# Kernel tuning notes

Measured on AMD Instinct MI355X. Metric: run time of the kernel, lower is better.

Reference implementation:

```python
import jax, jax.numpy as jnp
import numpy as np

DIM = 512
HEADS = 8
NUM_KEYS = 256
TOPK = 32
DIM_HEAD = 128
LN_EPS = 1e-5


def setup_inputs() -> dict:
    key = jax.random.key(0)
    k1, k2, k3, k4 = jax.random.split(key, 4)
    b, t = 2, 1024
    dim_query = DIM_HEAD * HEADS * 2
    x = jax.random.normal(k1, (b, t, DIM), dtype=jnp.float32)
    # nn.Linear(dim, dim_query, bias=False): weight (dim_query, dim), default kaiming-ish; use scaled normal
    Wq = jax.random.normal(k2, (dim_query, DIM), dtype=jnp.float32) / np.sqrt(DIM)
    # keys: (heads, num_keys, 2, dim_head), std = 1/sqrt(dim_head)
    keys = jax.random.normal(k3, (HEADS, NUM_KEYS, 2, DIM_HEAD), dtype=jnp.float32) / np.sqrt(DIM_HEAD)
    # values: (num_keys**2, dim), std = 1/sqrt(dim)
    values = jax.random.normal(k4, (NUM_KEYS ** 2, DIM), dtype=jnp.float32) / np.sqrt(DIM)
    ln_gamma = jnp.ones((DIM_HEAD,), dtype=jnp.float32)
    ln_beta = jnp.zeros((DIM_HEAD,), dtype=jnp.float32)
    return {"x": x, "Wq": Wq, "keys": keys, "values": values,
            "ln_gamma": ln_gamma, "ln_beta": ln_beta}


def reference(x, Wq, keys, values, ln_gamma, ln_beta):
    b, t, _ = x.shape
    h, n, _, d = keys.shape  # (heads, num_keys, 2, dim_head)
    k = TOPK

    # queries: 'b t (p h d)' -> (b, t, 2, h, d)
    q = jnp.einsum('btc,qc->btq', x, Wq).reshape(b, t, 2, h, d)

    # LayerNorm over dim_head (use_layernorm=True path)
    mu = q.mean(axis=-1, keepdims=True)
    var = q.var(axis=-1, keepdims=True)
    q = (q - mu) * jax.lax.rsqrt(var + LN_EPS) * ln_gamma + ln_beta

    # dots: 'p b t h d, h n p d -> b t h p n'
    dots = jnp.einsum('btphd,hnpd->bthpn', q, keys)

    # top-k per sub-key half: (b, t, h, 2, k)
    scores, indices = jax.lax.top_k(dots, k)
    sx, sy = scores[..., 0, :], scores[..., 1, :]
    ix, iy = indices[..., 0, :], indices[..., 1, :]

    # outer combination -> (b, t, h, k*k)
    all_scores = (sx[..., :, None] + sy[..., None, :]).reshape(b, t, h, k * k)
    all_indices = (ix[..., :, None] * n + iy[..., None, :]).reshape(b, t, h, k * k)

    final_scores, final_idx = jax.lax.top_k(all_scores, k)  # (b, t, h, k)
    value_indices = jnp.take_along_axis(all_indices, final_idx, axis=-1)
    attn = jax.nn.softmax(final_scores, axis=-1)

    vi = value_indices.reshape(b * t, h * k)
    w = attn.reshape(b * t, h * k)

    # EmbeddingBag(mode='sum') with per-sample weights
    gathered = values[vi]                      # (bt, hk, dim)
    out = jnp.einsum('nkd,nk->nd', gathered, w)
    return out.reshape(b, t, -1)
```

## Files before the change

kernel.cpp:

```cpp
#include <hip/hip_runtime.h>
#include <math.h>

#define DQ 2048
#define CDIM 512
#define NKEYS 256
#define KSEL 32

__device__ __forceinline__ bool rank_before(float as, int ai, float bs, int bi) {
  return (as > bs) || (as == bs && ai < bi);
}
static __device__ __forceinline__ float bf2f(unsigned int u) {
  union { unsigned int i; float f; } v; v.i = u << 16; return v.f;
}
static __device__ __forceinline__ unsigned int f2bf(float f) {
  union { float f; unsigned int i; } v; v.f = f;
  unsigned int r = v.i + 0x7fffu + ((v.i >> 16) & 1u);
  return r >> 16;
}

__device__ __forceinline__ void qgemm_body(
    const float* __restrict__ X, const float* __restrict__ W,
    const float* __restrict__ gamma, const float* __restrict__ beta,
    float* __restrict__ Q, float* smem, int bx, int by, int tid) {
  float* As = smem;
  float* Bs = smem + 16 * 68;
  const int m0 = bx * 64, n0 = by * 128;
  const int tx = tid & 15, ty = tid >> 4;
  const int am = tid >> 2, ak = (tid & 3) * 4;
  const int bn = tid >> 1, bk = (tid & 1) * 8;
  float acc[4][8] = {};
  float4 av  = *(const float4*)&X[(size_t)(m0 + am) * CDIM + ak];
  float4 bv0 = *(const float4*)&W[(size_t)(n0 + bn) * CDIM + bk];
  float4 bv1 = *(const float4*)&W[(size_t)(n0 + bn) * CDIM + bk + 4];
  for (int kt = 0; kt < CDIM; kt += 16) {
    __syncthreads();
    As[(ak + 0) * 68 + am] = av.x; As[(ak + 1) * 68 + am] = av.y;
    As[(ak + 2) * 68 + am] = av.z; As[(ak + 3) * 68 + am] = av.w;
    Bs[(bk + 0) * 132 + bn] = bv0.x; Bs[(bk + 1) * 132 + bn] = bv0.y;
    Bs[(bk + 2) * 132 + bn] = bv0.z; Bs[(bk + 3) * 132 + bn] = bv0.w;
    Bs[(bk + 4) * 132 + bn] = bv1.x; Bs[(bk + 5) * 132 + bn] = bv1.y;
    Bs[(bk + 6) * 132 + bn] = bv1.z; Bs[(bk + 7) * 132 + bn] = bv1.w;
    __syncthreads();
    if (kt + 16 < CDIM) {
      av  = *(const float4*)&X[(size_t)(m0 + am) * CDIM + kt + 16 + ak];
      bv0 = *(const float4*)&W[(size_t)(n0 + bn) * CDIM + kt + 16 + bk];
      bv1 = *(const float4*)&W[(size_t)(n0 + bn) * CDIM + kt + 16 + bk + 4];
    }
    #pragma unroll
    for (int kk = 0; kk < 16; ++kk) {
      float4 a4  = *(const float4*)&As[kk * 68 + ty * 4];
      float4 b4a = *(const float4*)&Bs[kk * 132 + tx * 8];
      float4 b4b = *(const float4*)&Bs[kk * 132 + tx * 8 + 4];
      const float ar[4] = {a4.x, a4.y, a4.z, a4.w};
      const float br[8] = {b4a.x, b4a.y, b4a.z, b4a.w, b4b.x, b4b.y, b4b.z, b4b.w};
      #pragma unroll
      for (int i = 0; i < 4; ++i)
        #pragma unroll
        for (int j = 0; j < 8; ++j)
          acc[i][j] += ar[i] * br[j];
    }
  }
  float g[8], bta[8];
  #pragma unroll
  for (int j = 0; j < 8; ++j) { g[j] = gamma[tx * 8 + j]; bta[j] = beta[tx * 8 + j]; }
  #pragma unroll
  for (int i = 0; i < 4; ++i) {
    float s = 0.f, sq = 0.f;
    #pragma unroll
    for (int j = 0; j < 8; ++j) { s += acc[i][j]; sq += acc[i][j] * acc[i][j]; }
    #pragma unroll
    for (int m = 1; m < 16; m <<= 1) {
      s += __shfl_xor(s, m, 64);
      sq += __shfl_xor(sq, m, 64);
    }
    float mean = s * (1.0f / 128.0f);
    float var = sq * (1.0f / 128.0f) - mean * mean;
    float rs = 1.0f / sqrtf(var + 1e-5f);
    float o[8];
    #pragma unroll
    for (int j = 0; j < 8; ++j) o[j] = (acc[i][j] - mean) * rs * g[j] + bta[j];
    float* dst = &Q[(size_t)(m0 + ty * 4 + i) * DQ + n0 + tx * 8];
    *(float4*)dst = make_float4(o[0], o[1], o[2], o[3]);
    *(float4*)(dst + 4) = make_float4(o[4], o[5], o[6], o[7]);
  }
}

__device__ __forceinline__ void transpose_body(
    const float* __restrict__ keys, float* __restrict__ keysT,
    float* smem, int hp, int ny, int tid) {
  float* tile = smem;
  const int h = hp >> 1, p = hp & 1;
  const int n0 = ny * 64;
  {
    const int n = tid >> 2;
    const int d0 = (tid & 3) * 32;
    const float* src = &keys[(((size_t)h * NKEYS + n0 + n) * 2 + p) * 128 + d0];
    #pragma unroll
    for (int j = 0; j < 32; j += 4) {
      float4 v = *(const float4*)(src + j);
      tile[n * 129 + d0 + j + 0] = v.x;
      tile[n * 129 + d0 + j + 1] = v.y;
      tile[n * 129 + d0 + j + 2] = v.z;
      tile[n * 129 + d0 + j + 3] = v.w;
    }
  }
  __syncthreads();
  {
    const int d = tid >> 1;
    const int nh = (tid & 1) * 32;
    float* dst = &keysT[((size_t)hp * 128 + d) * NKEYS + n0 + nh];
    #pragma unroll
    for (int j = 0; j < 32; j += 4) {
      float4 o = make_float4(tile[(nh + j + 0) * 129 + d], tile[(nh + j + 1) * 129 + d],
                             tile[(nh + j + 2) * 129 + d], tile[(nh + j + 3) * 129 + d]);
      *(float4*)(dst + j) = o;
    }
  }
}

__device__ __forceinline__ void convert_body(
    const float* __restrict__ values, unsigned int* __restrict__ vbf, int cb, int tid) {
  const size_t g = ((size_t)cb * 256 + tid) * 8;
  float4 a = *(const float4*)(values + g);
  float4 b = *(const float4*)(values + g + 4);
  uint4 pk;
  pk.x = f2bf(a.x) | (f2bf(a.y) << 16);
  pk.y = f2bf(a.z) | (f2bf(a.w) << 16);
  pk.z = f2bf(b.x) | (f2bf(b.y) << 16);
  pk.w = f2bf(b.z) | (f2bf(b.w) << 16);
  *(uint4*)(vbf + g / 2) = pk;
}

__global__ __launch_bounds__(256) void fused_pre(
    const float* __restrict__ X, const float* __restrict__ W,
    const float* __restrict__ gamma, const float* __restrict__ beta,
    float* __restrict__ Q,
    const float* __restrict__ keys, float* __restrict__ keysT,
    const float* __restrict__ values, unsigned int* __restrict__ vbf) {
  __shared__ float smem[64 * 129];
  const int b = blockIdx.x;
  const int tid = threadIdx.x;
  if (b < 512) {
    qgemm_body(X, W, gamma, beta, Q, smem, b & 31, b >> 5, tid);
  } else if (b < 576) {
    const int idx = b - 512;
    transpose_body(keys, keysT, smem, idx & 15, idx >> 4, tid);
  } else {
    convert_body(values, vbf, b - 576, tid);
  }
}

__global__ __launch_bounds__(256) void qgemm_ln(
    const float* __restrict__ X, const float* __restrict__ W,
    const float* __restrict__ gamma, const float* __restrict__ beta,
    float* __restrict__ Q) {
  __shared__ float smem[16 * 68 + 16 * 132];
  qgemm_body(X, W, gamma, beta, Q, smem, blockIdx.x, blockIdx.y, threadIdx.x);
}

__global__ __launch_bounds__(256) void transpose_keys(
    const float* __restrict__ keys, float* __restrict__ keysT) {
  __shared__ float smem[64 * 129];
  transpose_body(keys, keysT, smem, blockIdx.x, blockIdx.y, threadIdx.x);
}

__global__ __launch_bounds__(256) void convert_values(
    const float* __restrict__ values, unsigned int* __restrict__ vbf) {
  convert_body(values, vbf, blockIdx.x, threadIdx.x);
}

__global__ __launch_bounds__(512, 5) void dots_sel(
    const float* __restrict__ Q, const float* __restrict__ keysT,
    float* __restrict__ s1s, int* __restrict__ s1i) {
  const int hp = blockIdx.x;
  const int chunk = blockIdx.y;
  const int h = hp >> 1, p = hp & 1;
  const int t0 = chunk * 32;
  const int tid = threadIdx.x;
  const int w = tid >> 6, lane = tid & 63;
  const int wu = __builtin_amdgcn_readfirstlane(w);
  const float* q0 = &Q[(size_t)(t0 + wu * 4 + 0) * DQ + p * 1024 + h * 128];
  const float* q1 = q0 + DQ;
  const float* q2 = q0 + 2 * DQ;
  const float* q3 = q0 + 3 * DQ;
  const float* kT = keysT + (size_t)hp * 128 * NKEYS + lane * 4;
  float acc[4][4] = {};
  #pragma unroll 2
  for (int kt = 0; kt < 128; kt += 4) {
    float4 a0 = *(const float4*)&q0[kt];
    float4 a1 = *(const float4*)&q1[kt];
    float4 a2 = *(const float4*)&q2[kt];
    float4 a3 = *(const float4*)&q3[kt];
    const float a0r[4] = {a0.x, a0.y, a0.z, a0.w};
    const float a1r[4] = {a1.x, a1.y, a1.z, a1.w};
    const float a2r[4] = {a2.x, a2.y, a2.z, a2.w};
    const float a3r[4] = {a3.x, a3.y, a3.z, a3.w};
    #pragma unroll
    for (int kk = 0; kk < 4; ++kk) {
      float4 b4 = *(const float4*)&kT[(size_t)(kt + kk) * NKEYS];
      const float br[4] = {b4.x, b4.y, b4.z, b4.w};
      #pragma unroll
      for (int j = 0; j < 4; ++j) {
        acc[0][j] += a0r[kk] * br[j];
        acc[1][j] += a1r[kk] * br[j];
        acc[2][j] += a2r[kk] * br[j];
        acc[3][j] += a3r[kk] * br[j];
      }
    }
  }
  #define CE1(S, I, a, b, dd)                                                  \
    {                                                                          \
      bool sw_ = (dd) ? rank_before(S[a], I[a], S[b], I[b])                    \
                      : rank_before(S[b], I[b], S[a], I[a]);                   \
      if (sw_) {                                                               \
        float ts_ = S[a]; S[a] = S[b]; S[b] = ts_;                             \
        int ti_ = I[a]; I[a] = I[b]; I[b] = ti_;                               \
      }                                                                        \
    }
  #define CEP(a, b, dd) { CE1(sA, iA, a, b, dd) CE1(sB, iB, a, b, dd) }
  #define CROSSP(L, dd)                                                        \
    {                                                                          \
      bool amHigh = (lane & (L)) != 0;                                         \
      bool flip = amHigh != (dd);                                              \
      _Pragma("unroll")                                                        \
      for (int r = 0; r < 4; ++r) {                                            \
        float osA = __shfl_xor(sA[r], (L), 64);                                \
        int oiA = __shfl_xor(iA[r], (L), 64);                                  \
        float osB = __shfl_xor(sB[r], (L), 64);                                \
        int oiB = __shfl_xor(iB[r], (L), 64);                                  \
        bool tA = rank_before(osA, oiA, sA[r], iA[r]) != flip;                 \
        if (tA) { sA[r] = osA; iA[r] = oiA; }                                  \
        bool tB = rank_before(osB, oiB, sB[r], iB[r]) != flip;                 \
        if (tB) { sB[r] = osB; iB[r] = oiB; }                                  \
      }                                                                        \
    }
  #pragma unroll
  for (int ii = 0; ii < 4; ii += 2) {
    float sA[4], sB[4]; int iA[4], iB[4];
    #pragma unroll
    for (int r = 0; r < 4; ++r) {
      sA[r] = acc[ii][r];     iA[r] = lane * 4 + r;
      sB[r] = acc[ii + 1][r]; iB[r] = lane * 4 + r;
    }
    CEP(0, 1, false); CEP(2, 3, true);
    {
      bool dd = (lane & 1) != 0;
      CEP(0, 2, dd); CEP(1, 3, dd); CEP(0, 1, dd); CEP(2, 3, dd);
    }
    #pragma unroll
    for (int K = 8; K <= 256; K <<= 1) {
      bool dd = (lane & (K >> 2)) != 0;
      #pragma unroll
      for (int L = K >> 3; L >= 1; L >>= 1) CROSSP(L, dd);
      CEP(0, 2, dd); CEP(1, 3, dd); CEP(0, 1, dd); CEP(2, 3, dd);
    }
    const int instA = (t0 + w * 4 + ii) * 16 + hp;
    const int instB = instA + 16;
    if (lane < 8) {
      *(float4*)&s1s[(size_t)instA * KSEL + lane * 4] = make_float4(sA[0], sA[1], sA[2], sA[3]);
      *(int4*)&s1i[(size_t)instA * KSEL + lane * 4] = make_int4(iA[0], iA[1], iA[2], iA[3]);
      *(float4*)&s1s[(size_t)instB * KSEL + lane * 4] = make_float4(sB[0], sB[1], sB[2], sB[3]);
      *(int4*)&s1i[(size_t)instB * KSEL + lane * 4] = make_int4(iB[0], iB[1], iB[2], iB[3]);
    }
  }
  #undef CE1
  #undef CEP
  #undef CROSSP
}

__constant__ unsigned short slot_ij[128] = {
  0,1,2,3,4,5,6,7,8,9,10,11,12,13,14,15,16,17,18,19,20,21,22,23,24,25,26,27,28,29,30,31,
  32,33,34,35,36,37,38,39,40,41,42,43,44,45,46,47,
  64,65,66,67,68,69,70,71,72,73,
  96,97,98,99,100,101,102,103,
  128,129,130,131,132,133,
  160,161,162,163,164,
  192,193,194,195,
  224,225,226,227,
  256,257,258,
  288,289,290,
  320,321, 352,353, 384,385, 416,417, 448,449, 480,481,
  512,544,576,608,640,672,704,736,768,800,832,864,896,928,960,992,
  0xFFFF,0xFFFF,0xFFFF,0xFFFF,0xFFFF,0xFFFF,0xFFFF,0xFFFF,0xFFFF
};

__global__ __launch_bounds__(256) void stage2_gather(
    const float* __restrict__ s1s, const int* __restrict__ s1i,
    const unsigned short* __restrict__ vbf, float* __restrict__ out) {
  const int t = blockIdx.x;
  const int tid = threadIdx.x, w = tid >> 6, lane = tid & 63;
  __shared__ float ws_[256];
  __shared__ int vs_[256];
  __shared__ float part[4 * 520];
  {
    const int thA = t * 8 + w * 2;
    const int bxA = thA * 64, byA = bxA + 32;
    const int bxB = bxA + 64, byB = bxA + 96;
    float sA[2], sB[2]; int idA[2], idB[2];
    #pragma unroll
    for (int r = 0; r < 2; ++r) {
      int sl = slot_ij[lane * 2 + r];
      if (sl != 0xFFFF) {
        sA[r] = s1s[bxA + (sl >> 5)] + s1s[byA + (sl & 31)];
        sB[r] = s1s[bxB + (sl >> 5)] + s1s[byB + (sl & 31)];
        idA[r] = sl; idB[r] = sl;
      } else {
        sA[r] = -INFINITY; idA[r] = 0x7fffffff;
        sB[r] = -INFINITY; idB[r] = 0x7fffffff;
      }
    }
    #define CE2I(S, I, dd)                                                     \
      {                                                                        \
        bool sw = (dd) ? rank_before(S[0], I[0], S[1], I[1])                   \
                       : rank_before(S[1], I[1], S[0], I[0]);                  \
        if (sw) {                                                              \
          float ts = S[0]; S[0] = S[1]; S[1] = ts;                             \
          int ti = I[0]; I[0] = I[1]; I[1] = ti;                               \
        }                                                                      \
      }
    #define CE2P(dd) { CE2I(sA, idA, dd) CE2I(sB, idB, dd) }
    #define CROSS2P(L, dd)                                                     \
      {                                                                        \
        bool amHigh = (lane & (L)) != 0;                                       \
        bool flip = amHigh != (dd);                                            \
        _Pragma("unroll")                                                      \
        for (int r = 0; r < 2; ++r) {                                          \
          float osA = __shfl_xor(sA[r], (L), 64);                              \
          int oiA = __shfl_xor(idA[r], (L), 64);                               \
          float osB = __shfl_xor(sB[r], (L), 64);                              \
          int oiB = __shfl_xor(idB[r], (L), 64);                               \
          bool tA = rank_before(osA, oiA, sA[r], idA[r]) != flip;              \
          if (tA) { sA[r] = osA; idA[r] = oiA; }                               \
          bool tB = rank_before(osB, oiB, sB[r], idB[r]) != flip;              \
          if (tB) { sB[r] = osB; idB[r] = oiB; }                               \
        }                                                                      \
      }
    { bool dd = (lane & 1) != 0; CE2P(dd); }
    #pragma unroll
    for (int K = 4; K <= 128; K <<= 1) {
      bool dd = (lane & (K >> 1)) != 0;
      #pragma unroll
      for (int L = K >> 2; L >= 1; L >>= 1) CROSS2P(L, dd);
      CE2P(dd);
    }
    #undef CE2I
    #undef CE2P
    #undef CROSS2P
    float smA = __shfl(sA[0], 0, 64);
    float smB = __shfl(sB[0], 0, 64);
    float eA0 = 0.f, eA1 = 0.f, eB0 = 0.f, eB1 = 0.f;
    if (lane < 16) {
      eA0 = expf(sA[0] - smA); eA1 = expf(sA[1] - smA);
      eB0 = expf(sB[0] - smB); eB1 = expf(sB[1] - smB);
    }
    float pA = eA0 + eA1, pB = eB0 + eB1;
    #pragma unroll
    for (int m = 1; m < 16; m <<= 1) {
      pA += __shfl_xor(pA, m, 64);
      pB += __shfl_xor(pB, m, 64);
    }
    if (lane < 16) {
      const int fA0 = idA[0], fA1 = idA[1], fB0 = idB[0], fB1 = idB[1];
      const int viA0 = s1i[bxA + (fA0 >> 5)] * NKEYS + s1i[byA + (fA0 & 31)];
      const int viA1 = s1i[bxA + (fA1 >> 5)] * NKEYS + s1i[byA + (fA1 & 31)];
      const int viB0 = s1i[bxB + (fB0 >> 5)] * NKEYS + s1i[byB + (fB0 & 31)];
      const int viB1 = s1i[bxB + (fB1 >> 5)] * NKEYS + s1i[byB + (fB1 & 31)];
      const int eoA = (w * 2) * 32 + lane * 2;
      const int eoB = eoA + 32;
      ws_[eoA] = eA0 / pA; ws_[eoA + 1] = eA1 / pA;
      vs_[eoA] = viA0;     vs_[eoA + 1] = viA1;
      ws_[eoB] = eB0 / pB; ws_[eoB + 1] = eB1 / pB;
      vs_[eoB] = viB0;     vs_[eoB + 1] = viB1;
    }
  }
  __syncthreads();
  float acc[8] = {};
  const int c0 = lane * 8;
  #pragma unroll 1
  for (int phase = 0; phase < 4; ++phase) {
    for (int e = w; e < 256; e += 4) {
      const int row = vs_[e];
      if ((row >> 14) != phase) continue;
      const float wv = ws_[e];
      uint4 pk = *(const uint4*)(vbf + (size_t)row * CDIM + c0);
      acc[0] += wv * bf2f(pk.x & 0xffff); acc[1] += wv * bf2f(pk.x >> 16);
      acc[2] += wv * bf2f(pk.y & 0xffff); acc[3] += wv * bf2f(pk.y >> 16);
      acc[4] += wv * bf2f(pk.z & 0xffff); acc[5] += wv * bf2f(pk.z >> 16);
      acc[6] += wv * bf2f(pk.w & 0xffff); acc[7] += wv * bf2f(pk.w >> 16);
    }
  }
  #pragma unroll
  for (int j = 0; j < 8; j += 4)
    *(float4*)&part[w * 520 + c0 + j] =
        make_float4(acc[j], acc[j + 1], acc[j + 2], acc[j + 3]);
  __syncthreads();
  const int c2 = tid * 2;
  float r0 = part[c2] + part[520 + c2] + part[1040 + c2] + part[1560 + c2];
  float r1 = part[c2 + 1] + part[520 + c2 + 1] + part[1040 + c2 + 1] + part[1560 + c2 + 1];
  *(float2*)(out + (size_t)t * CDIM + c2) = make_float2(r0, r1);
}

__global__ __launch_bounds__(256) void stage2_kernel(
    const float* __restrict__ s1s, const int* __restrict__ s1i,
    float* __restrict__ wgt, int* __restrict__ vidx) {
  const int th = blockIdx.x * 4 + (threadIdx.x >> 6);
  const int lane = threadIdx.x & 63;
  const int bx = th * 64;
  const int by = bx + 32;
  float s[2]; int id[2];
  #pragma unroll
  for (int r = 0; r < 2; ++r) {
    int sl = slot_ij[lane * 2 + r];
    if (sl != 0xFFFF) {
      s[r] = s1s[bx + (sl >> 5)] + s1s[by + (sl & 31)];
      id[r] = sl;
    } else {
      s[r] = -INFINITY; id[r] = 0x7fffffff;
    }
  }
  #define CE2(dd)                                                              \
    {                                                                          \
      bool sw = (dd) ? rank_before(s[0], id[0], s[1], id[1])                   \
                     : rank_before(s[1], id[1], s[0], id[0]);                  \
      if (sw) {                                                                \
        float ts = s[0]; s[0] = s[1]; s[1] = ts;                               \
        int ti = id[0]; id[0] = id[1]; id[1] = ti;                             \
      }                                                                        \
    }
  #define CROSS2(L, dd)                                                        \
    {                                                                          \
      bool amHigh = (lane & (L)) != 0;                                         \
      bool flip = amHigh != (dd);                                              \
      _Pragma("unroll")                                                        \
      for (int r = 0; r < 2; ++r) {                                            \
        float os = __shfl_xor(s[r], (L), 64);                                  \
        int oi = __shfl_xor(id[r], (L), 64);                                   \
        bool take = rank_before(os, oi, s[r], id[r]) != flip;                  \
        if (take) { s[r] = os; id[r] = oi; }                                   \
      }                                                                        \
    }
  { bool dd = (lane & 1) != 0; CE2(dd); }
  #pragma unroll
  for (int K = 4; K <= 128; K <<= 1) {
    bool dd = (lane & (K >> 1)) != 0;
    #pragma unroll
    for (int L = K >> 2; L >= 1; L >>= 1) CROSS2(L, dd);
    CE2(dd);
  }
  #undef CE2
  #undef CROSS2
  float smax = __shfl(s[0], 0, 64);
  float e0 = 0.f, e1 = 0.f;
  if (lane < 16) { e0 = expf(s[0] - smax); e1 = expf(s[1] - smax); }
  float part = e0 + e1;
  #pragma unroll
  for (int m = 1; m < 16; m <<= 1) part += __shfl_xor(part, m, 64);
  if (lane < 16) {
    int f0 = id[0], f1 = id[1];
    int vi0 = s1i[bx + (f0 >> 5)] * NKEYS + s1i[by + (f0 & 31)];
    int vi1 = s1i[bx + (f1 >> 5)] * NKEYS + s1i[by + (f1 & 31)];
    wgt[(size_t)th * KSEL + lane * 2] = e0 / part;
    wgt[(size_t)th * KSEL + lane * 2 + 1] = e1 / part;
    vidx[(size_t)th * KSEL + lane * 2] = vi0;
    vidx[(size_t)th * KSEL + lane * 2 + 1] = vi1;
  }
}

__global__ __launch_bounds__(256) void gather_kernel(
    const float* __restrict__ wgt, const int* __restrict__ vidx,
    const float* __restrict__ values, float* __restrict__ out) {
  const int tp = blockIdx.x;
  const int tid = threadIdx.x;
  __shared__ float ws_[512];
  __shared__ int vs_[512];
  ws_[tid] = wgt[(size_t)tp * 512 + tid];
  ws_[tid + 256] = wgt[(size_t)tp * 512 + tid + 256];
  vs_[tid] = vidx[(size_t)tp * 512 + tid];
  vs_[tid + 256] = vidx[(size_t)tp * 512 + tid + 256];
  __syncthreads();
  const int sub = tid >> 7;
  const int c4 = (tid & 127) * 4;
  const float* wp = &ws_[sub * 256];
  const int* vp = &vs_[sub * 256];
  float4 a = make_float4(0.f, 0.f, 0.f, 0.f);
  #pragma unroll 4
  for (int e = 0; e < 256; ++e) {
    float4 vv = *(const float4*)(values + (size_t)vp[e] * CDIM + c4);
    float wv = wp[e];
    a.x += wv * vv.x; a.y += wv * vv.y; a.z += wv * vv.z; a.w += wv * vv.w;
  }
  *(float4*)(out + (size_t)(tp * 2 + sub) * CDIM + c4) = a;
}

extern "C" void kernel_launch(void* const* d_in, const int* in_sizes, int n_in,
                              void* d_out, int out_size, void* d_ws, size_t ws_size,
                              hipStream_t stream) {
  const float* X      = (const float*)d_in[0];
  const float* W      = (const float*)d_in[1];
  const float* keys   = (const float*)d_in[2];
  const float* values = (const float*)d_in[3];
  const float* gamma  = (const float*)d_in[4];
  const float* beta   = (const float*)d_in[5];
  char* ws = (char*)d_ws;

  if (ws_size >= (92u << 20)) {
    float* s1s = (float*)(ws);
    int*   s1i = (int*)  (ws + (4u << 20));
    float* kT  = (float*)(ws + (8u << 20));
    unsigned int* vbf = (unsigned int*)(ws + (12u << 20));
    float* Q   = (float*)(ws + (76u << 20));
    fused_pre<<<16960, 256, 0, stream>>>(X, W, gamma, beta, Q, keys, kT, values, vbf);
    dots_sel<<<dim3(16, 64), 512, 0, stream>>>(Q, kT, s1s, s1i);
    stage2_gather<<<2048, 256, 0, stream>>>(s1s, s1i, (const unsigned short*)vbf, (float*)d_out);
  } else {
    float* s1s = (float*)(ws);
    int*   s1i = (int*)  (ws + (4u << 20));
    float* wgt = (float*)(ws + (8u << 20));
    int*   vix = (int*)  (ws + (10u << 20));
    float* Q   = (float*)(ws + (12u << 20));
    float* kT  = (float*)(ws + (28u << 20));
    unsigned int* vbf = (unsigned int*)(ws + (12u << 20));
    const bool bf16_path = ws_size >= (76u << 20);
    transpose_keys<<<dim3(16, 4), 256, 0, stream>>>(keys, kT);
    qgemm_ln<<<dim3(32, 16), 256, 0, stream>>>(X, W, gamma, beta, Q);
    dots_sel<<<dim3(16, 64), 512, 0, stream>>>(Q, kT, s1s, s1i);
    if (bf16_path) {
      convert_values<<<16384, 256, 0, stream>>>(values, vbf);
      stage2_gather<<<2048, 256, 0, stream>>>(s1s, s1i, (const unsigned short*)vbf, (float*)d_out);
    } else {
      stage2_kernel<<<4096, 256, 0, stream>>>(s1s, s1i, wgt, vix);
      gather_kernel<<<1024, 256, 0, stream>>>(wgt, vix, values, (float*)d_out);
    }
  }
}
```

Baseline: 402.6 us.

## Pre-transpose Wq and replace LDS-tiled query GEMM with register-blocked direct-load GEMM

Adds a prep kernel that transposes the key tensor and also the projection weight Wq into workspace. The query GEMM plus LayerNorm is rewritten without LDS: each wave reads rows of X directly, reads contiguous float4 columns of the transposed weight, and does the LayerNorm reduction with wave shuffles. The values-to-bf16 conversion moves into the same 512-thread kernel. This costs an extra kernel launch and a weight transpose, and it relies on cache reuse of X and WT in place of shared-memory tiling.

```diff
diff --git a/kernel.cpp b/kernel.cpp
--- a/kernel.cpp
+++ b/kernel.cpp
@@ -118,9 +118,149 @@
   }
 }
 
-__device__ __forceinline__ void convert_body(
-    const float* __restrict__ values, unsigned int* __restrict__ vbf, int cb, int tid) {
-  const size_t g = ((size_t)cb * 256 + tid) * 8;
+__device__ __forceinline__ void wtrans_body(
+    const float* __restrict__ W, float* __restrict__ WT, float* smem, int b, int tid) {
+  float* tile = smem;
+  const int qi = b >> 3, ci = b & 7;
+  const int q0 = qi * 64, c0 = ci * 64;
+  {
+    const int r = tid >> 2;
+    const int cc = (tid & 3) * 16;
+    const float* src = &W[(size_t)(q0 + r) * CDIM + c0 + cc];
+    #pragma unroll
+    for (int j = 0; j < 16; j += 4) {
+      float4 v = *(const float4*)(src + j);
+      tile[r * 65 + cc + j + 0] = v.x;
+      tile[r * 65 + cc + j + 1] = v.y;
+      tile[r * 65 + cc + j + 2] = v.z;
+      tile[r * 65 + cc + j + 3] = v.w;
+    }
+  }
+  __syncthreads();
+  {
+    const int c = tid >> 2;
+    const int rr = (tid & 3) * 16;
+    float* dst = &WT[(size_t)(c0 + c) * DQ + q0 + rr];
+    #pragma unroll
+    for (int j = 0; j < 16; j += 4) {
+      float4 o = make_float4(tile[(rr + j + 0) * 65 + c], tile[(rr + j + 1) * 65 + c],
+                             tile[(rr + j + 2) * 65 + c], tile[(rr + j + 3) * 65 + c]);
+      *(float4*)(dst + j) = o;
+    }
+  }
+}
+
+__device__ __forceinline__ void qgemm_nolds_body(
+    const float* __restrict__ X, const float* __restrict__ WT,
+    const float* __restrict__ gamma, const float* __restrict__ beta,
+    float* __restrict__ Q, int b, int tid) {
+  const int bx = b >> 3;
+  const int by = b & 7;
+  const int w = tid >> 6, lane = tid & 63;
+  const int wu = __builtin_amdgcn_readfirstlane(w);
+  const int r0 = bx * 32 + wu * 4;
+  const int n0 = by * 256;
+  const float* x0 = &X[(size_t)r0 * CDIM];
+  const float* x1 = x0 + CDIM;
+  const float* x2 = x0 + 2 * CDIM;
+  const float* x3 = x0 + 3 * CDIM;
+  const float* wt = WT + n0 + lane * 4;
+  float acc[4][4] = {};
+  #pragma unroll 2
+  for (int kt = 0; kt < CDIM; kt += 4) {
+    float4 a0 = *(const float4*)&x0[kt];
+    float4 a1 = *(const float4*)&x1[kt];
+    float4 a2 = *(const float4*)&x2[kt];
+    float4 a3 = *(const float4*)&x3[kt];
+    const float a0r[4] = {a0.x, a0.y, a0.z, a0.w};
+    const float a1r[4] = {a1.x, a1.y, a1.z, a1.w};
+    const float a2r[4] = {a2.x, a2.y, a2.z, a2.w};
+    const float a3r[4] = {a3.x, a3.y, a3.z, a3.w};
+    #pragma unroll
+    for (int kk = 0; kk < 4; ++kk) {
+      float4 b4 = *(const float4*)&wt[(size_t)(kt + kk) * DQ];
+      const float br[4] = {b4.x, b4.y, b4.z, b4.w};
+      #pragma unroll
+      for (int j = 0; j < 4; ++j) {
+        acc[0][j] += a0r[kk] * br[j];
+        acc[1][j] += a1r[kk] * br[j];
+        acc[2][j] += a2r[kk] * br[j];
+        acc[3][j] += a3r[kk] * br[j];
+      }
+    }
+  }
+  float g[4], bta[4];
+  const int gi = (lane & 31) * 4;
+  #pragma unroll
+  for (int j = 0; j < 4; ++j) { g[j] = gamma[gi + j]; bta[j] = beta[gi + j]; }
+  const int rw = bx * 32 + w * 4;
+  #pragma unroll
+  for (int i = 0; i < 4; ++i) {
+    float s = 0.f, sq = 0.f;
+    #pragma unroll
+    for (int j = 0; j < 4; ++j) { s += acc[i][j]; sq += acc[i][j] * acc[i][j]; }
+    #pragma unroll
+    for (int m = 1; m < 32; m <<= 1) {
+      s += __shfl_xor(s, m, 64);
+      sq += __shfl_xor(sq, m, 64);
+    }
+    float mean = s * (1.0f / 128.0f);
+    float var = sq * (1.0f / 128.0f) - mean * mean;
+    float rs = 1.0f / sqrtf(var + 1e-5f);
+    float o[4];
+    #pragma unroll
+    for (int j = 0; j < 4; ++j) o[j] = (acc[i][j] - mean) * rs * g[j] + bta[j];
+    *(float4*)&Q[(size_t)(rw + i) * DQ + n0 + lane * 4] = make_float4(o[0], o[1], o[2], o[3]);
+  }
+}
+
+__global__ __launch_bounds__(256) void prep(
+    const float* __restrict__ keys, float* __restrict__ keysT,
+    const float* __restrict__ W, float* __restrict__ WT) {
+  __shared__ float smem[64 * 129];
+  const int b = blockIdx.x, tid = threadIdx.x;
+  if (b < 64) transpose_body(keys, keysT, smem, b & 15, b >> 4, tid);
+  else wtrans_body(W, WT, smem, b - 64, tid);
+}
+
+__global__ __launch_bounds__(512) void fused_mid(
+    const float* __restrict__ X, const float* __restrict__ WT,
+    const float* __restrict__ gamma, const float* __restrict__ beta,
+    float* __restrict__ Q,
+    const float* __restrict__ values, unsigned int* __restrict__ vbf) {
+  const int b = blockIdx.x, tid = threadIdx.x;
+  if (b < 512) {
+    qgemm_nolds_body(X, WT, gamma, beta, Q, b, tid);
+  } else {
+    const size_t g = ((size_t)(b - 512) * 512 + tid) * 8;
+    float4 a = *(const float4*)(values + g);
+    float4 c = *(const float4*)(values + g + 4);
+    uint4 pk;
+    pk.x = f2bf(a.x) | (f2bf(a.y) << 16);
+    pk.y = f2bf(a.z) | (f2bf(a.w) << 16);
+    pk.z = f2bf(c.x) | (f2bf(c.y) << 16);
+    pk.w = f2bf(c.z) | (f2bf(c.w) << 16);
+    *(uint4*)(vbf + g / 2) = pk;
+  }
+}
+
+__global__ __launch_bounds__(256) void qgemm_ln(
+    const float* __restrict__ X, const float* __restrict__ W,
+    const float* __restrict__ gamma, const float* __restrict__ beta,
+    float* __restrict__ Q) {
+  __shared__ float smem[16 * 68 + 16 * 132];
+  qgemm_body(X, W, gamma, beta, Q, smem, blockIdx.x, blockIdx.y, threadIdx.x);
+}
+
+__global__ __launch_bounds__(256) void transpose_keys(
+    const float* __restrict__ keys, float* __restrict__ keysT) {
+  __shared__ float smem[64 * 129];
+  transpose_body(keys, keysT, smem, blockIdx.x, blockIdx.y, threadIdx.x);
+}
+
+__global__ __launch_bounds__(256) void convert_values(
+    const float* __restrict__ values, unsigned int* __restrict__ vbf) {
+  const size_t g = ((size_t)blockIdx.x * 256 + threadIdx.x) * 8;
   float4 a = *(const float4*)(values + g);
   float4 b = *(const float4*)(values + g + 4);
   uint4 pk;
@@ -129,44 +269,6 @@
   pk.z = f2bf(b.x) | (f2bf(b.y) << 16);
   pk.w = f2bf(b.z) | (f2bf(b.w) << 16);
   *(uint4*)(vbf + g / 2) = pk;
-}
-
-__global__ __launch_bounds__(256) void fused_pre(
-    const float* __restrict__ X, const float* __restrict__ W,
-    const float* __restrict__ gamma, const float* __restrict__ beta,
-    float* __restrict__ Q,
-    const float* __restrict__ keys, float* __restrict__ keysT,
-    const float* __restrict__ values, unsigned int* __restrict__ vbf) {
-  __shared__ float smem[64 * 129];
-  const int b = blockIdx.x;
-  const int tid = threadIdx.x;
-  if (b < 512) {
-    qgemm_body(X, W, gamma, beta, Q, smem, b & 31, b >> 5, tid);
-  } else if (b < 576) {
-    const int idx = b - 512;
-    transpose_body(keys, keysT, smem, idx & 15, idx >> 4, tid);
-  } else {
-    convert_body(values, vbf, b - 576, tid);
-  }
-}
-
-__global__ __launch_bounds__(256) void qgemm_ln(
-    const float* __restrict__ X, const float* __restrict__ W,
-    const float* __restrict__ gamma, const float* __restrict__ beta,
-    float* __restrict__ Q) {
-  __shared__ float smem[16 * 68 + 16 * 132];
-  qgemm_body(X, W, gamma, beta, Q, smem, blockIdx.x, blockIdx.y, threadIdx.x);
-}
-
-__global__ __launch_bounds__(256) void transpose_keys(
-    const float* __restrict__ keys, float* __restrict__ keysT) {
-  __shared__ float smem[64 * 129];
-  transpose_body(keys, keysT, smem, blockIdx.x, blockIdx.y, threadIdx.x);
-}
-
-__global__ __launch_bounds__(256) void convert_values(
-    const float* __restrict__ values, unsigned int* __restrict__ vbf) {
-  convert_body(values, vbf, blockIdx.x, threadIdx.x);
 }
 
 __global__ __launch_bounds__(512, 5) void dots_sel(
@@ -505,11 +607,13 @@
 
   if (ws_size >= (92u << 20)) {
     float* s1s = (float*)(ws);
+    float* WT  = (float*)(ws);
     int*   s1i = (int*)  (ws + (4u << 20));
     float* kT  = (float*)(ws + (8u << 20));
     unsigned int* vbf = (unsigned int*)(ws + (12u << 20));
     float* Q   = (float*)(ws + (76u << 20));
-    fused_pre<<<16960, 256, 0, stream>>>(X, W, gamma, beta, Q, keys, kT, values, vbf);
+    prep<<<320, 256, 0, stream>>>(keys, kT, W, WT);
+    fused_mid<<<8704, 512, 0, stream>>>(X, WT, gamma, beta, Q, values, vbf);
     dots_sel<<<dim3(16, 64), 512, 0, stream>>>(Q, kT, s1s, s1i);
     stage2_gather<<<2048, 256, 0, stream>>>(s1s, s1i, (const unsigned short*)vbf, (float*)d_out);
   } else {
```

New measurement: 452.2 us. 12.3% more time.
